# Kernel optimization log

Measured on AMD Instinct MI355X. Metric: run time of the kernel, lower is better.

Reference implementation:

```python
import jax, jax.numpy as jnp
import numpy as np

B, S, H = 128, 512, 1024  # batch, max_len, hidden=output=encoder dim

def setup_inputs() -> dict:
    key = jax.random.key(0)
    ks = jax.random.split(key, 8)
    sc = 0.02
    return {
        "input_seq": jax.random.normal(ks[0], (B, H), jnp.float32),
        "last_hidden": jax.random.normal(ks[1], (1, B, H), jnp.float32),
        "encoder_outputs": jax.random.normal(ks[2], (S, B, H), jnp.float32),
        "W_ih": jax.random.normal(ks[3], (3 * H, H), jnp.float32) * sc,
        "b_ih": jnp.zeros((3 * H,), jnp.float32),
        "W_hh": jax.random.normal(ks[4], (3 * H, H), jnp.float32) * sc,
        "b_hh": jnp.zeros((3 * H,), jnp.float32),
        "W_attn": jax.random.normal(ks[5], (H, H), jnp.float32) * sc,
        "b_attn": jnp.zeros((H,), jnp.float32),
        "W_concat": jax.random.normal(ks[6], (H, 2 * H), jnp.float32) * sc,
        "b_concat": jnp.zeros((H,), jnp.float32),
        "W_out": jax.random.normal(ks[7], (H, H), jnp.float32) * sc,
        "b_out": jnp.zeros((H,), jnp.float32),
    }

def reference(input_seq, last_hidden, encoder_outputs,
              W_ih, b_ih, W_hh, b_hh,
              W_attn, b_attn, W_concat, b_concat, W_out, b_out):
    h = last_hidden[0]                                # [B,H]
    # --- single GRU step (PyTorch gate order r,z,n) ---
    gi = input_seq @ W_ih.T + b_ih                    # [B,3H]
    gh = h @ W_hh.T + b_hh                            # [B,3H]
    i_r, i_z, i_n = jnp.split(gi, 3, axis=-1)
    h_r, h_z, h_n = jnp.split(gh, 3, axis=-1)
    r = jax.nn.sigmoid(i_r + h_r)
    z = jax.nn.sigmoid(i_z + h_z)
    n = jnp.tanh(i_n + r * h_n)
    rnn_output = (1.0 - z) * n + z * h                # [B,H]
    hidden = rnn_output[None]                         # [1,B,H]
    # --- 'general' attention, vectorized over (b, i) ---
    proj = jnp.einsum('sbd,hd->sbh', encoder_outputs, W_attn) + b_attn  # [S,B,H]
    energies = jnp.einsum('bh,sbh->bs', rnn_output, proj)               # [B,S]
    attn_weights = jax.nn.softmax(energies, axis=-1)[:, None, :]        # [B,1,S]
    # --- context + output head ---
    context = jnp.einsum('bs,sbd->bd', attn_weights[:, 0, :], encoder_outputs)  # [B,H]
    concat_input = jnp.concatenate([rnn_output, context], axis=1)       # [B,2H]
    concat_output = jnp.tanh(concat_input @ W_concat.T + b_concat)      # [B,H]
    output = jax.nn.sigmoid(concat_output @ W_out.T + b_out)            # [B,H]
    return (output, hidden, attn_weights)
```

## Files before the change

kernel.cpp:

```cpp
#include <hip/hip_runtime.h>
#include <cstddef>

#define B_ 128
#define H_ 1024
#define S_ 512


__device__ __forceinline__ void stage_A128(float* As, const float* __restrict__ A, int k0, int tid){
  int c4 = tid & 15, rowg = tid >> 4;
#pragma unroll
  for (int p = 0; p < 8; ++p){
    int row = p*16 + rowg;
    const float4 v = *reinterpret_cast<const float4*>(A + (size_t)row*H_ + k0 + c4*4);
    int colx = row ^ ((c4 & 7) << 2);
    float* d0 = As + (c4*4)*132 + colx;
    d0[0]     = v.x;
    d0[132]   = v.y;
    d0[264]   = v.z;
    d0[396]   = v.w;
  }
}

__device__ __forceinline__ void stage_W_wt(float* Ws, const float* __restrict__ W, int n0, int k0, int ldw, int tid){
  int n = tid >> 4, c4 = tid & 15;
  const float4 v = *reinterpret_cast<const float4*>(W + (size_t)(n0+n)*ldw + k0 + c4*4);
  *reinterpret_cast<float4*>(Ws + n*68 + c4*4) = v;
}

__device__ __forceinline__ void stage_W_wn(float* Ws, const float* __restrict__ W, int n0, int k0, int ldw, int tid){
  int k = tid >> 2, c4 = tid & 3;
  const float4 v = *reinterpret_cast<const float4*>(W + (size_t)(k0+k)*ldw + n0 + c4*4);
  Ws[(c4*4+0)*68 + k] = v.x;
  Ws[(c4*4+1)*68 + k] = v.y;
  Ws[(c4*4+2)*68 + k] = v.z;
  Ws[(c4*4+3)*68 + k] = v.w;
}

__device__ __forceinline__ void compute_chunk(const float* As, const float* Ws, int tb, int tn, float acc[4][2]){
#pragma unroll
  for (int kk = 0; kk < 64; kk += 4){
    int col = (4*tb) ^ (((kk >> 2) & 7) << 2);
    float av[4][4];
#pragma unroll
    for (int k = 0; k < 4; ++k)
      *reinterpret_cast<float4*>(av[k]) = *reinterpret_cast<const float4*>(As + (kk+k)*132 + col);
    float w0[4], w1[4];
    *reinterpret_cast<float4*>(w0) = *reinterpret_cast<const float4*>(Ws + (tn*2+0)*68 + kk);
    *reinterpret_cast<float4*>(w1) = *reinterpret_cast<const float4*>(Ws + (tn*2+1)*68 + kk);
#pragma unroll
    for (int k = 0; k < 4; ++k){
#pragma unroll
      for (int i = 0; i < 4; ++i){
        acc[i][0] = fmaf(av[k][i], w0[k], acc[i][0]);
        acc[i][1] = fmaf(av[k][i], w1[k], acc[i][1]);
      }
    }
  }
}

__global__ __launch_bounds__(256) void gru_gemm(const float* __restrict__ Ain, const float* __restrict__ Ah,
                                                const float* __restrict__ Wih, const float* __restrict__ Whh,
                                                float* __restrict__ G){
  __shared__ float As[64*132];
  __shared__ float Ws[16*68];
  int tid = threadIdx.x;
  int n0g = blockIdx.x * 16;
  int kbase = blockIdx.y * 512;
  const float* A; const float* W; int n0;
  if (n0g < 3072){ A = Ain; W = Wih; n0 = n0g; }
  else           { A = Ah;  W = Whh; n0 = n0g - 3072; }
  int tb = tid & 31, tn = tid >> 5;
  float acc[4][2] = {{0.f,0.f},{0.f,0.f},{0.f,0.f},{0.f,0.f}};
  for (int kq = 0; kq < 512; kq += 64){
    int k0 = kbase + kq;
    __syncthreads();
    stage_A128(As, A, k0, tid);
    stage_W_wt(Ws, W, n0, k0, H_, tid);
    __syncthreads();
    compute_chunk(As, Ws, tb, tn, acc);
  }
  float* Gp = G + (size_t)blockIdx.y * 786432;
#pragma unroll
  for (int i = 0; i < 4; ++i){
    int b = tb*4 + i;
#pragma unroll
    for (int j = 0; j < 2; ++j){
      int n = tn*2 + j;
      Gp[(size_t)b*6144 + n0g + n] = acc[i][j];
    }
  }
}

template<int KSUB, bool WT, bool ASPLIT>
__global__ __launch_bounds__(256) void gemm_partial(const float* __restrict__ A1, const float* __restrict__ A2,
                                                    const float* __restrict__ W, int ldw,
                                                    float* __restrict__ partial){
  __shared__ float As[64*132];
  __shared__ float Ws[16*68];
  int tid = threadIdx.x;
  int n0 = blockIdx.x * 16;
  int kbase = blockIdx.y * KSUB;
  int tb = tid & 31, tn = tid >> 5;
  float acc[4][2] = {{0.f,0.f},{0.f,0.f},{0.f,0.f},{0.f,0.f}};
  for (int kq = 0; kq < KSUB; kq += 64){
    int k0 = kbase + kq;
    const float* A = A1; int keff = k0;
    if (ASPLIT && k0 >= 1024){ A = A2; keff = k0 - 1024; }
    __syncthreads();
    stage_A128(As, A, keff, tid);
    if (WT) stage_W_wt(Ws, W, n0, k0, ldw, tid);
    else    stage_W_wn(Ws, W, n0, k0, ldw, tid);
    __syncthreads();
    compute_chunk(As, Ws, tb, tn, acc);
  }
  float* P = partial + (size_t)blockIdx.y * (B_*H_);
#pragma unroll
  for (int i = 0; i < 4; ++i){
    int b = tb*4 + i;
#pragma unroll
    for (int j = 0; j < 2; ++j){
      int n = tn*2 + j;
      P[(size_t)b*1024 + n0 + n] = acc[i][j];
    }
  }
}

template<int ACT, int NP>
__global__ __launch_bounds__(256) void combine(const float* __restrict__ partial, const float* __restrict__ bias,
                                               float* __restrict__ C){
  int idx = blockIdx.x*256 + threadIdx.x;
  float v = 0.f;
#pragma unroll
  for (int j = 0; j < NP; ++j) v += partial[(size_t)j*(B_*H_) + idx];
  if (bias) v += bias[idx & 1023];
  if (ACT == 1) v = tanhf(v);
  if (ACT == 2) v = 1.f/(1.f + expf(-v));
  C[idx] = v;
}

__global__ __launch_bounds__(1024) void gru_gates(const float* __restrict__ G, const float* __restrict__ h,
                                                  const float* __restrict__ bih, const float* __restrict__ bhh,
                                                  const float* __restrict__ ba,
                                                  float* __restrict__ rnn, float* __restrict__ hid_out,
                                                  float* __restrict__ t){
  int b = blockIdx.x, c = threadIdx.x;
  __shared__ float red[16];
  const float* g0 = G + (size_t)b*6144;
  const float* g1 = G + 786432 + (size_t)b*6144;
  float ir  = g0[c]      + g1[c]      + bih[c];
  float iz  = g0[c+1024] + g1[c+1024] + bih[c+1024];
  float in_ = g0[c+2048] + g1[c+2048] + bih[c+2048];
  float hr  = g0[c+3072] + g1[c+3072] + bhh[c];
  float hz  = g0[c+4096] + g1[c+4096] + bhh[c+1024];
  float hn  = g0[c+5120] + g1[c+5120] + bhh[c+2048];
  float r = 1.f/(1.f + expf(-(ir + hr)));
  float z = 1.f/(1.f + expf(-(iz + hz)));
  float n = tanhf(in_ + r*hn);
  float hv = h[(size_t)b*H_ + c];
  float o = (1.f - z)*n + z*hv;
  rnn[(size_t)b*H_ + c] = o;
  hid_out[(size_t)b*H_ + c] = o;
  float s = o * ba[c];
#pragma unroll
  for (int off = 1; off < 64; off <<= 1) s += __shfl_xor(s, off, 64);
  if ((c & 63) == 0) red[c >> 6] = s;
  __syncthreads();
  if (c == 0){
    float acc = 0.f;
#pragma unroll
    for (int j = 0; j < 16; ++j) acc += red[j];
    t[b] = acc;
  }
}

__global__ __launch_bounds__(256) void attn_pass(const float* __restrict__ enc, const float* __restrict__ q,
                                                 const float* __restrict__ t, float* __restrict__ e_out,
                                                 float* __restrict__ ctxp, float* __restrict__ mw){
  int b = blockIdx.x;
  int chunk = blockIdx.y;
  int wave = threadIdx.x >> 6;
  int lane = threadIdx.x & 63;
  int s0 = chunk*64 + wave*16;

  float qv[4][4];
#pragma unroll
  for (int k = 0; k < 4; ++k)
    *reinterpret_cast<float4*>(qv[k]) = *reinterpret_cast<const float4*>(q + (size_t)b*H_ + k*256 + lane*4);
  const float tb = t[b];

  float m = -INFINITY;
  float ctx[4][4] = {{0}};
  const float* rowp = enc + ((size_t)s0 * B_ + b) * H_;
  float rv[4][4];
#pragma unroll
  for (int k = 0; k < 4; ++k)
    *reinterpret_cast<float4*>(rv[k]) = *reinterpret_cast<const float4*>(rowp + k*256 + lane*4);

  for (int i = 0; i < 16; ++i){
    float nv[4][4];
    if (i < 15){
      const float* np = rowp + (size_t)B_*H_;
#pragma unroll
      for (int k = 0; k < 4; ++k)
        *reinterpret_cast<float4*>(nv[k]) = *reinterpret_cast<const float4*>(np + k*256 + lane*4);
    }
    float p = 0.f;
#pragma unroll
    for (int k = 0; k < 4; ++k)
#pragma unroll
      for (int j = 0; j < 4; ++j) p = fmaf(rv[k][j], qv[k][j], p);
#pragma unroll
    for (int off = 1; off < 64; off <<= 1) p += __shfl_xor(p, off, 64);
    float e = p + tb;
    if (lane == 0) e_out[(size_t)b*S_ + s0 + i] = e;
    float mn = fmaxf(m, e);
    float sc = expf(m - mn);
    float w  = expf(e - mn);
#pragma unroll
    for (int k = 0; k < 4; ++k)
#pragma unroll
      for (int j = 0; j < 4; ++j) ctx[k][j] = fmaf(w, rv[k][j], ctx[k][j]*sc);
    m = mn;
    rowp += (size_t)B_*H_;
    if (i < 15){
#pragma unroll
      for (int k = 0; k < 4; ++k)
#pragma unroll
        for (int j = 0; j < 4; ++j) rv[k][j] = nv[k][j];
    }
  }
  int pidx = b*32 + chunk*4 + wave;
  float* cp = ctxp + (size_t)pidx*H_;
#pragma unroll
  for (int k = 0; k < 4; ++k)
    *reinterpret_cast<float4*>(cp + k*256 + lane*4) = *reinterpret_cast<const float4*>(ctx[k]);
  if (lane == 0) mw[pidx] = m;
}

__global__ __launch_bounds__(256) void softmax_combine(const float* __restrict__ e, const float* __restrict__ mw,
                                                       const float* __restrict__ ctxp, float* __restrict__ attn_out,
                                                       float* __restrict__ ctx){
  int b = blockIdx.x;
  int tid = threadIdx.x;
  __shared__ float red[4];
  __shared__ float Msh, Lsh;
  __shared__ float scs[32];
  float e0 = e[(size_t)b*S_ + tid];
  float e1 = e[(size_t)b*S_ + 256 + tid];
  float mx = fmaxf(e0, e1);
#pragma unroll
  for (int off = 1; off < 64; off <<= 1) mx = fmaxf(mx, __shfl_xor(mx, off, 64));
  if ((tid & 63) == 0) red[tid >> 6] = mx;
  __syncthreads();
  if (tid == 0) Msh = fmaxf(fmaxf(red[0], red[1]), fmaxf(red[2], red[3]));
  __syncthreads();
  float M = Msh;
  float w0 = expf(e0 - M), w1 = expf(e1 - M);
  float ls = w0 + w1;
#pragma unroll
  for (int off = 1; off < 64; off <<= 1) ls += __shfl_xor(ls, off, 64);
  if ((tid & 63) == 0) red[tid >> 6] = ls;
  __syncthreads();
  if (tid == 0) Lsh = red[0] + red[1] + red[2] + red[3];
  __syncthreads();
  float Linv = 1.0f / Lsh;
  attn_out[(size_t)b*S_ + tid]       = w0 * Linv;
  attn_out[(size_t)b*S_ + 256 + tid] = w1 * Linv;
  if (tid < 32) scs[tid] = expf(mw[b*32 + tid] - M) * Linv;
  __syncthreads();
#pragma unroll
  for (int it = 0; it < 4; ++it){
    int d = it*256 + tid;
    float acc = 0.f;
#pragma unroll
    for (int j = 0; j < 32; ++j) acc = fmaf(scs[j], ctxp[(size_t)(b*32 + j)*H_ + d], acc);
    ctx[(size_t)b*H_ + d] = acc;
  }
}

extern "C" void kernel_launch(void* const* d_in, const int* in_sizes, int n_in,
                              void* d_out, int out_size, void* d_ws, size_t ws_size,
                              hipStream_t stream){
  (void)in_sizes; (void)n_in; (void)out_size; (void)ws_size;
  const float* input_seq = (const float*)d_in[0];
  const float* last_hid  = (const float*)d_in[1];
  const float* enc       = (const float*)d_in[2];
  const float* W_ih      = (const float*)d_in[3];
  const float* b_ih      = (const float*)d_in[4];
  const float* W_hh      = (const float*)d_in[5];
  const float* b_hh      = (const float*)d_in[6];
  const float* W_attn    = (const float*)d_in[7];
  const float* b_attn    = (const float*)d_in[8];
  const float* W_concat  = (const float*)d_in[9];
  const float* b_concat  = (const float*)d_in[10];
  const float* W_out     = (const float*)d_in[11];
  const float* b_out     = (const float*)d_in[12];

  float* out = (float*)d_out;
  float* ws  = (float*)d_ws;

  float* G    = ws;
  float* rnn  = ws + 1572864;
  float* q    = ws + 1703936;
  float* t    = ws + 1835008;
  float* e    = ws + 1835136;
  float* mw   = ws + 1900672;
  float* ctx  = ws + 1904768;
  float* co   = ws + 2035840;
  float* part = ws + 2166912;
  float* ctxp = ws + 2691200;

  dim3 blk(256);
  gru_gemm<<<dim3(384,2), blk, 0, stream>>>(input_seq, last_hid, W_ih, W_hh, G);
  gru_gates<<<128, dim3(1024), 0, stream>>>(G, last_hid, b_ih, b_hh, b_attn, rnn, out + 131072, t);
  gemm_partial<256, false, false><<<dim3(64,4), blk, 0, stream>>>(rnn, nullptr, W_attn, 1024, part);
  combine<0, 4><<<512, blk, 0, stream>>>(part, nullptr, q);
  attn_pass<<<dim3(128, 8), blk, 0, stream>>>(enc, q, t, e, ctxp, mw);
  softmax_combine<<<128, blk, 0, stream>>>(e, mw, ctxp, out + 262144, ctx);
  gemm_partial<512, true, true><<<dim3(64,4), blk, 0, stream>>>(rnn, ctx, W_concat, 2048, part);
  combine<1, 4><<<512, blk, 0, stream>>>(part, b_concat, co);
  gemm_partial<256, true, false><<<dim3(64,4), blk, 0, stream>>>(co, nullptr, W_out, 1024, part);
  combine<2, 4><<<512, blk, 0, stream>>>(part, b_out, out);
}
```

Before: 546.5 us.

## Split K across waves with larger register tiles and fold q combine into attention

GEMM kernels now assign each wave a 16-wide k slice and give each thread an 8x4 output tile with padded shared layouts, which lowers shared-memory loads per FMA. Each wave writes its own partial, so the number of partial buffers grows fourfold and the gate, combine and attention kernels sum 8 or 16 partials. The separate combine for the attention query is removed and attn_pass reduces the 16 q partials itself. The cost is extra global traffic and workspace for the partials.

```diff
diff --git a/kernel.cpp b/kernel.cpp
--- a/kernel.cpp
+++ b/kernel.cpp
@@ -6,88 +6,87 @@
 #define S_ 512
 
 
-__device__ __forceinline__ void stage_A128(float* As, const float* __restrict__ A, int k0, int tid){
+__device__ __forceinline__ int bpad(int b){ return b + ((b >> 4) << 2); }
+
+#define LDA 156
+#define LDW 20
+
+__device__ __forceinline__ void stage_A2(float* As, const float* __restrict__ A, int k0, int tid){
   int c4 = tid & 15, rowg = tid >> 4;
 #pragma unroll
   for (int p = 0; p < 8; ++p){
     int row = p*16 + rowg;
     const float4 v = *reinterpret_cast<const float4*>(A + (size_t)row*H_ + k0 + c4*4);
-    int colx = row ^ ((c4 & 7) << 2);
-    float* d0 = As + (c4*4)*132 + colx;
-    d0[0]     = v.x;
-    d0[132]   = v.y;
-    d0[264]   = v.z;
-    d0[396]   = v.w;
-  }
-}
-
-__device__ __forceinline__ void stage_W_wt(float* Ws, const float* __restrict__ W, int n0, int k0, int ldw, int tid){
+    float* d = As + (c4*4)*LDA + bpad(row);
+    d[0]     = v.x;
+    d[LDA]   = v.y;
+    d[2*LDA] = v.z;
+    d[3*LDA] = v.w;
+  }
+}
+
+__device__ __forceinline__ void stage_Wt_wt(float* Wt, const float* __restrict__ W, int n0, int k0, int ldw, int tid){
   int n = tid >> 4, c4 = tid & 15;
   const float4 v = *reinterpret_cast<const float4*>(W + (size_t)(n0+n)*ldw + k0 + c4*4);
-  *reinterpret_cast<float4*>(Ws + n*68 + c4*4) = v;
-}
-
-__device__ __forceinline__ void stage_W_wn(float* Ws, const float* __restrict__ W, int n0, int k0, int ldw, int tid){
+  float* d = Wt + (c4*4)*LDW + n;
+  d[0]     = v.x;
+  d[LDW]   = v.y;
+  d[2*LDW] = v.z;
+  d[3*LDW] = v.w;
+}
+
+__device__ __forceinline__ void stage_Wt_wn(float* Wt, const float* __restrict__ W, int n0, int k0, int ldw, int tid){
   int k = tid >> 2, c4 = tid & 3;
   const float4 v = *reinterpret_cast<const float4*>(W + (size_t)(k0+k)*ldw + n0 + c4*4);
-  Ws[(c4*4+0)*68 + k] = v.x;
-  Ws[(c4*4+1)*68 + k] = v.y;
-  Ws[(c4*4+2)*68 + k] = v.z;
-  Ws[(c4*4+3)*68 + k] = v.w;
-}
-
-__device__ __forceinline__ void compute_chunk(const float* As, const float* Ws, int tb, int tn, float acc[4][2]){
-#pragma unroll
-  for (int kk = 0; kk < 64; kk += 4){
-    int col = (4*tb) ^ (((kk >> 2) & 7) << 2);
-    float av[4][4];
-#pragma unroll
-    for (int k = 0; k < 4; ++k)
-      *reinterpret_cast<float4*>(av[k]) = *reinterpret_cast<const float4*>(As + (kk+k)*132 + col);
-    float w0[4], w1[4];
-    *reinterpret_cast<float4*>(w0) = *reinterpret_cast<const float4*>(Ws + (tn*2+0)*68 + kk);
-    *reinterpret_cast<float4*>(w1) = *reinterpret_cast<const float4*>(Ws + (tn*2+1)*68 + kk);
-#pragma unroll
-    for (int k = 0; k < 4; ++k){
-#pragma unroll
-      for (int i = 0; i < 4; ++i){
-        acc[i][0] = fmaf(av[k][i], w0[k], acc[i][0]);
-        acc[i][1] = fmaf(av[k][i], w1[k], acc[i][1]);
-      }
-    }
+  *reinterpret_cast<float4*>(Wt + k*LDW + c4*4) = v;
+}
+
+__device__ __forceinline__ void compute_chunk2(const float* As, const float* Wt, int wave, int bp0, int ng,
+                                               float acc[8][4]){
+#pragma unroll
+  for (int kk = 0; kk < 16; ++kk){
+    int k = wave*16 + kk;
+    const float* r = As + k*LDA;
+    float a[8], w[4];
+    *reinterpret_cast<float4*>(&a[0]) = *reinterpret_cast<const float4*>(r + bp0);
+    *reinterpret_cast<float4*>(&a[4]) = *reinterpret_cast<const float4*>(r + bp0 + 4);
+    *reinterpret_cast<float4*>(&w[0]) = *reinterpret_cast<const float4*>(Wt + k*LDW + ng*4);
+#pragma unroll
+    for (int i = 0; i < 8; ++i)
+#pragma unroll
+      for (int j = 0; j < 4; ++j)
+        acc[i][j] = fmaf(a[i], w[j], acc[i][j]);
   }
 }
 
 __global__ __launch_bounds__(256) void gru_gemm(const float* __restrict__ Ain, const float* __restrict__ Ah,
                                                 const float* __restrict__ Wih, const float* __restrict__ Whh,
                                                 float* __restrict__ G){
-  __shared__ float As[64*132];
-  __shared__ float Ws[16*68];
+  __shared__ float As[64*LDA];
+  __shared__ float Wt[64*LDW];
   int tid = threadIdx.x;
   int n0g = blockIdx.x * 16;
   int kbase = blockIdx.y * 512;
   const float* A; const float* W; int n0;
   if (n0g < 3072){ A = Ain; W = Wih; n0 = n0g; }
   else           { A = Ah;  W = Whh; n0 = n0g - 3072; }
-  int tb = tid & 31, tn = tid >> 5;
-  float acc[4][2] = {{0.f,0.f},{0.f,0.f},{0.f,0.f},{0.f,0.f}};
+  int wave = tid >> 6, lane = tid & 63;
+  int bg = lane & 15, ng = lane >> 4;
+  int b0 = bg*8, bp0 = bpad(b0);
+  float acc[8][4] = {};
   for (int kq = 0; kq < 512; kq += 64){
     int k0 = kbase + kq;
     __syncthreads();
-    stage_A128(As, A, k0, tid);
-    stage_W_wt(Ws, W, n0, k0, H_, tid);
+    stage_A2(As, A, k0, tid);
+    stage_Wt_wt(Wt, W, n0, k0, H_, tid);
     __syncthreads();
-    compute_chunk(As, Ws, tb, tn, acc);
-  }
-  float* Gp = G + (size_t)blockIdx.y * 786432;
-#pragma unroll
-  for (int i = 0; i < 4; ++i){
-    int b = tb*4 + i;
-#pragma unroll
-    for (int j = 0; j < 2; ++j){
-      int n = tn*2 + j;
-      Gp[(size_t)b*6144 + n0g + n] = acc[i][j];
-    }
+    compute_chunk2(As, Wt, wave, bp0, ng, acc);
+  }
+  float* Gp = G + (size_t)(blockIdx.y*4 + wave) * 786432;
+#pragma unroll
+  for (int i = 0; i < 8; ++i){
+    float4 v = make_float4(acc[i][0], acc[i][1], acc[i][2], acc[i][3]);
+    *reinterpret_cast<float4*>(Gp + (size_t)(b0+i)*6144 + n0g + ng*4) = v;
   }
 }
 
@@ -95,43 +94,41 @@
 __global__ __launch_bounds__(256) void gemm_partial(const float* __restrict__ A1, const float* __restrict__ A2,
                                                     const float* __restrict__ W, int ldw,
                                                     float* __restrict__ partial){
-  __shared__ float As[64*132];
-  __shared__ float Ws[16*68];
+  __shared__ float As[64*LDA];
+  __shared__ float Wt[64*LDW];
   int tid = threadIdx.x;
   int n0 = blockIdx.x * 16;
   int kbase = blockIdx.y * KSUB;
-  int tb = tid & 31, tn = tid >> 5;
-  float acc[4][2] = {{0.f,0.f},{0.f,0.f},{0.f,0.f},{0.f,0.f}};
+  int wave = tid >> 6, lane = tid & 63;
+  int bg = lane & 15, ng = lane >> 4;
+  int b0 = bg*8, bp0 = bpad(b0);
+  float acc[8][4] = {};
   for (int kq = 0; kq < KSUB; kq += 64){
     int k0 = kbase + kq;
     const float* A = A1; int keff = k0;
     if (ASPLIT && k0 >= 1024){ A = A2; keff = k0 - 1024; }
     __syncthreads();
-    stage_A128(As, A, keff, tid);
-    if (WT) stage_W_wt(Ws, W, n0, k0, ldw, tid);
-    else    stage_W_wn(Ws, W, n0, k0, ldw, tid);
+    stage_A2(As, A, keff, tid);
+    if (WT) stage_Wt_wt(Wt, W, n0, k0, ldw, tid);
+    else    stage_Wt_wn(Wt, W, n0, k0, ldw, tid);
     __syncthreads();
-    compute_chunk(As, Ws, tb, tn, acc);
-  }
-  float* P = partial + (size_t)blockIdx.y * (B_*H_);
-#pragma unroll
-  for (int i = 0; i < 4; ++i){
-    int b = tb*4 + i;
-#pragma unroll
-    for (int j = 0; j < 2; ++j){
-      int n = tn*2 + j;
-      P[(size_t)b*1024 + n0 + n] = acc[i][j];
-    }
-  }
-}
-
-template<int ACT, int NP>
+    compute_chunk2(As, Wt, wave, bp0, ng, acc);
+  }
+  float* P = partial + (size_t)(blockIdx.y*4 + wave) * (B_*H_);
+#pragma unroll
+  for (int i = 0; i < 8; ++i){
+    float4 v = make_float4(acc[i][0], acc[i][1], acc[i][2], acc[i][3]);
+    *reinterpret_cast<float4*>(P + (size_t)(b0+i)*1024 + n0 + ng*4) = v;
+  }
+}
+
+template<int ACT>
 __global__ __launch_bounds__(256) void combine(const float* __restrict__ partial, const float* __restrict__ bias,
                                                float* __restrict__ C){
   int idx = blockIdx.x*256 + threadIdx.x;
   float v = 0.f;
 #pragma unroll
-  for (int j = 0; j < NP; ++j) v += partial[(size_t)j*(B_*H_) + idx];
+  for (int j = 0; j < 16; ++j) v += partial[(size_t)j*(B_*H_) + idx];
   if (bias) v += bias[idx & 1023];
   if (ACT == 1) v = tanhf(v);
   if (ACT == 2) v = 1.f/(1.f + expf(-v));
@@ -145,14 +142,14 @@
                                                   float* __restrict__ t){
   int b = blockIdx.x, c = threadIdx.x;
   __shared__ float red[16];
-  const float* g0 = G + (size_t)b*6144;
-  const float* g1 = G + 786432 + (size_t)b*6144;
-  float ir  = g0[c]      + g1[c]      + bih[c];
-  float iz  = g0[c+1024] + g1[c+1024] + bih[c+1024];
-  float in_ = g0[c+2048] + g1[c+2048] + bih[c+2048];
-  float hr  = g0[c+3072] + g1[c+3072] + bhh[c];
-  float hz  = g0[c+4096] + g1[c+4096] + bhh[c+1024];
-  float hn  = g0[c+5120] + g1[c+5120] + bhh[c+2048];
+  float ir = bih[c], iz = bih[c+1024], in_ = bih[c+2048];
+  float hr = bhh[c], hz = bhh[c+1024], hn  = bhh[c+2048];
+#pragma unroll
+  for (int p = 0; p < 8; ++p){
+    const float* g = G + (size_t)p*786432 + (size_t)b*6144;
+    ir  += g[c];      iz += g[c+1024]; in_ += g[c+2048];
+    hr  += g[c+3072]; hz += g[c+4096]; hn  += g[c+5120];
+  }
   float r = 1.f/(1.f + expf(-(ir + hr)));
   float z = 1.f/(1.f + expf(-(iz + hz)));
   float n = tanhf(in_ + r*hn);
@@ -173,7 +170,7 @@
   }
 }
 
-__global__ __launch_bounds__(256) void attn_pass(const float* __restrict__ enc, const float* __restrict__ q,
+__global__ __launch_bounds__(256) void attn_pass(const float* __restrict__ enc, const float* __restrict__ qpart,
                                                  const float* __restrict__ t, float* __restrict__ e_out,
                                                  float* __restrict__ ctxp, float* __restrict__ mw){
   int b = blockIdx.x;
@@ -184,8 +181,15 @@
 
   float qv[4][4];
 #pragma unroll
-  for (int k = 0; k < 4; ++k)
-    *reinterpret_cast<float4*>(qv[k]) = *reinterpret_cast<const float4*>(q + (size_t)b*H_ + k*256 + lane*4);
+  for (int k = 0; k < 4; ++k){
+    float4 s = make_float4(0.f,0.f,0.f,0.f);
+#pragma unroll
+    for (int p = 0; p < 16; ++p){
+      const float4 v = *reinterpret_cast<const float4*>(qpart + (size_t)p*(B_*H_) + (size_t)b*H_ + k*256 + lane*4);
+      s.x += v.x; s.y += v.y; s.z += v.z; s.w += v.w;
+    }
+    qv[k][0]=s.x; qv[k][1]=s.y; qv[k][2]=s.z; qv[k][3]=s.w;
+  }
   const float tb = t[b];
 
   float m = -INFINITY;
@@ -299,26 +303,25 @@
   float* out = (float*)d_out;
   float* ws  = (float*)d_ws;
 
-  float* G    = ws;
-  float* rnn  = ws + 1572864;
-  float* q    = ws + 1703936;
-  float* t    = ws + 1835008;
-  float* e    = ws + 1835136;
-  float* mw   = ws + 1900672;
-  float* ctx  = ws + 1904768;
-  float* co   = ws + 2035840;
-  float* part = ws + 2166912;
-  float* ctxp = ws + 2691200;
+  float* G     = ws;
+  float* rnn   = ws + 6291456;
+  float* t     = ws + 6422528;
+  float* e     = ws + 6422656;
+  float* mw    = ws + 6488192;
+  float* ctx   = ws + 6492288;
+  float* co    = ws + 6623360;
+  float* qpart = ws + 6754432;
+  float* part  = ws + 8851584;
+  float* ctxp  = ws + 10948736;
 
   dim3 blk(256);
   gru_gemm<<<dim3(384,2), blk, 0, stream>>>(input_seq, last_hid, W_ih, W_hh, G);
   gru_gates<<<128, dim3(1024), 0, stream>>>(G, last_hid, b_ih, b_hh, b_attn, rnn, out + 131072, t);
-  gemm_partial<256, false, false><<<dim3(64,4), blk, 0, stream>>>(rnn, nullptr, W_attn, 1024, part);
-  combine<0, 4><<<512, blk, 0, stream>>>(part, nullptr, q);
-  attn_pass<<<dim3(128, 8), blk, 0, stream>>>(enc, q, t, e, ctxp, mw);
+  gemm_partial<256, false, false><<<dim3(64,4), blk, 0, stream>>>(rnn, nullptr, W_attn, 1024, qpart);
+  attn_pass<<<dim3(128, 8), blk, 0, stream>>>(enc, qpart, t, e, ctxp, mw);
   softmax_combine<<<128, blk, 0, stream>>>(e, mw, ctxp, out + 262144, ctx);
   gemm_partial<512, true, true><<<dim3(64,4), blk, 0, stream>>>(rnn, ctx, W_concat, 2048, part);
-  combine<1, 4><<<512, blk, 0, stream>>>(part, b_concat, co);
+  combine<1><<<512, blk, 0, stream>>>(part, b_concat, co);
   gemm_partial<256, true, false><<<dim3(64,4), blk, 0, stream>>>(co, nullptr, W_out, 1024, part);
-  combine<2, 4><<<512, blk, 0, stream>>>(part, b_out, out);
-}
+  combine<2><<<512, blk, 0, stream>>>(part, b_out, out);
+}
```

After: 532.7 us. -2.5%, faster.
